# Performance work log

Measured on AMD Instinct MI355X. Metric: run time of the kernel, lower is better.

## Reference

```python
import jax, jax.numpy as jnp
import numpy as np

EPS = 1e-10


def _log_scaling(feats):
    """Raw feats (..., 15): xmin,ymin,xmax,ymax,area,angle,pca_big,pca_small,hu1..hu7
    -> (..., 17): xmin..area, log|pca_big..hu7|, lshape, cosangle, sinangle."""
    lshape = jnp.sqrt(feats[..., 7:8]) / (jnp.sqrt(feats[..., 6:7]) + EPS)
    cosangle = jnp.cos(feats[..., 5:6])
    sinangle = jnp.sin(feats[..., 5:6])
    logged = jnp.log(jnp.abs(feats[..., 5:]) + EPS)  # cols 5..14 logged
    # original drops the (logged) angle column 5 and keeps logged cols 6..14
    return jnp.concatenate([feats[..., :5], logged[..., 1:], lshape, cosangle, sinangle], axis=-1)


def _make_parents(n_trees, P, seed=0):
    """Valid topologically-ordered tree: parent[p] < p, parent[0] = 0 (root)."""
    rng = np.random.default_rng(seed)
    idx = np.arange(P)
    high = np.maximum(idx, 1)
    par = rng.integers(0, 2**31 - 1, size=(n_trees, P)) % high[None, :]
    par[:, 0] = 0
    return par.astype(np.int32)


def setup_inputs() -> dict:
    key = jax.random.key(0)
    k1, k2, k3, k4 = jax.random.split(key, 4)
    B, N, H, W = 2, 2, 1024, 1024
    P = H * W
    x = jax.random.normal(k1, (B, N, H, W), dtype=jnp.float32) * 10.0
    weight = jax.random.uniform(k2, (N, 17, 1), dtype=jnp.float32, minval=-0.01, maxval=0.01)
    bias = jnp.zeros((N, 1), dtype=jnp.float32)
    attrs = jax.random.uniform(k3, (B, N, P, 15), dtype=jnp.float32) * 4.0
    parents = jnp.asarray(_make_parents(B * N, P).reshape(B, N, P))
    return {"x": x, "weight": weight, "bias": bias, "attrs": attrs, "parents": parents}


def _path_sum(contrib_pad, par_pad, P):
    """Pointer-doubling root-to-node path sums over a tree with sentinel at index P."""
    iters = max(int(np.ceil(np.log2(max(P, 2)))), 1)

    def body(i, carry):
        v, p = carry
        return v + v[p], p[p]

    v, _ = jax.lax.fori_loop(0, iters, body, (contrib_pad, par_pad))
    return v[:P]


def reference(x, weight, bias, attrs, parents):
    B, N, H, W = x.shape
    P = H * W
    xf = x.reshape(B, N, P)
    idx = jnp.arange(P, dtype=parents.dtype)
    is_root = parents == idx  # (B,N,P)
    parent_vals = jnp.take_along_axis(xf, parents, axis=-1)
    diff = jnp.where(is_root, xf, xf - parent_vals)  # per-node gray-level increment
    feats = _log_scaling(attrs)  # (B,N,P,17)
    lin = jnp.einsum('bnpf,nfo->bnpo', feats, weight) + bias[None, :, None, :]
    scores = jax.nn.sigmoid(lin[..., 0])  # (B,N,P)
    contrib = diff * scores
    # sentinel node P with contribution 0; roots point at the sentinel
    sent = jnp.full((B, N, 1), P, dtype=parents.dtype)
    par_pad = jnp.concatenate([jnp.where(is_root, P, parents), sent], axis=-1)
    contrib_pad = jnp.concatenate([contrib, jnp.zeros((B, N, 1), x.dtype)], axis=-1)
    out = jax.vmap(jax.vmap(lambda c, p: _path_sum(c, p, P)))(contrib_pad, par_pad)
    return out.reshape(B, N, H, W)
```

## Files before the change

### kernel.cpp

```cpp
#include <hip/hip_runtime.h>
#include <math.h>

#define EPSF 1e-10f
#define P_NODES (1 << 20)
#define T_FRONT 65536
#define T_C1    262144
#define T_C2    524288

typedef float vf4 __attribute__((ext_vector_type(4)));
typedef float vf2 __attribute__((ext_vector_type(2)));

struct __align__(8) NodePair {
    float v;
    int   par;
};

__device__ __forceinline__ void tree_decomp(int b, int& tree, int& jj)
{
    tree = (b & 7) >> 1;
    jj   = ((b >> 3) << 1) | (b & 1);
}

__global__ __launch_bounds__(256) void score_kernel(
    const float* __restrict__ x,
    const float* __restrict__ weight,
    const float* __restrict__ bias,
    const float* __restrict__ attrs,
    const int*   __restrict__ parents,
    NodePair*    __restrict__ dst,
    int N)
{
    __shared__ float sA[256 * 15];

    const int t = threadIdx.x;
    int tree, jj;
    tree_decomp(blockIdx.x, tree, jj);
    const int blockBase = (tree << 20) + (jj << 8);
    const int idx = blockBase + t;

    const vf4* ab4 = (const vf4*)(attrs + (size_t)blockBase * 15);
    vf4* sA4 = (vf4*)sA;
#pragma unroll
    for (int k = t; k < 960; k += 256)
        sA4[k] = __builtin_nontemporal_load(&ab4[k]);

    const int n    = tree % N;
    const float* w = weight + n * 17;
    const float  b = bias[n];

    __syncthreads();

    const float* a = &sA[t * 15];

    float acc = b;
    acc += a[0] * w[0];
    acc += a[1] * w[1];
    acc += a[2] * w[2];
    acc += a[3] * w[3];
    acc += a[4] * w[4];

    const float a5 = a[5];
    const float a6 = a[6];
    const float a7 = a[7];

    acc += __logf(fabsf(a6)    + EPSF) * w[5];
    acc += __logf(fabsf(a7)    + EPSF) * w[6];
    acc += __logf(fabsf(a[8])  + EPSF) * w[7];
    acc += __logf(fabsf(a[9])  + EPSF) * w[8];
    acc += __logf(fabsf(a[10]) + EPSF) * w[9];
    acc += __logf(fabsf(a[11]) + EPSF) * w[10];
    acc += __logf(fabsf(a[12]) + EPSF) * w[11];
    acc += __logf(fabsf(a[13]) + EPSF) * w[12];
    acc += __logf(fabsf(a[14]) + EPSF) * w[13];

    const float lshape = __fsqrt_rn(a7) / (__fsqrt_rn(a6) + EPSF);
    acc += lshape * w[14];
    acc += __cosf(a5) * w[15];
    acc += __sinf(a5) * w[16];

    const float score = 1.0f / (1.0f + __expf(-acc));

    const int   p   = idx & (P_NODES - 1);
    const int   par = parents[idx];
    const float xv  = x[idx];

    NodePair r;
    if (par == p) {
        r.v   = xv * score;
        r.par = -1;
    } else {
        r.v   = (xv - x[(idx - p) + par]) * score;
        r.par = par;
    }
    dst[idx] = r;
}

__global__ __launch_bounds__(256) void frontier_kernel(
    const NodePair* __restrict__ pairs,
    float*          __restrict__ out)
{
    int tree, jj;
    tree_decomp(blockIdx.x, tree, jj);
    const int p    = (jj << 8) + threadIdx.x;
    const int base = tree << 20;
    const NodePair* tp = pairs + base;

    NodePair r = tp[p];
    float s = r.v;
    int   c = r.par;
    while (c >= 0) {
        NodePair q = tp[c];
        s += q.v;
        c  = q.par;
    }
    out[base + p] = s;
}

__global__ __launch_bounds__(256) void chunk_kernel(
    const NodePair* __restrict__ pairs,
    float*          __restrict__ out,
    int lo, int last)
{
    int tree, jj;
    tree_decomp(blockIdx.x, tree, jj);
    const int p0   = lo + ((((jj << 8) + threadIdx.x)) << 1);
    const int base = tree << 20;
    const NodePair* tp = pairs + base;

    float4 r = *(const float4*)(tp + p0);
    float s0 = r.x;  int c0 = __float_as_int(r.y);
    float s1 = r.z;  int c1 = __float_as_int(r.w);

    bool a0 = (c0 >= lo), a1 = (c1 >= lo);
    while (a0 || a1) {
        NodePair q0, q1;
        if (a0) q0 = tp[c0];
        if (a1) q1 = tp[c1];
        if (a0) { s0 += q0.v; c0 = q0.par; a0 = (c0 >= lo); }
        if (a1) { s1 += q1.v; c1 = q1.par; a1 = (c1 >= lo); }
    }
    s0 += out[base + c0];
    s1 += out[base + c1];

    vf2 o; o.x = s0; o.y = s1;
    if (last)
        __builtin_nontemporal_store(o, (vf2*)(out + base + p0));
    else
        *(vf2*)(out + base + p0) = o;
}

extern "C" void kernel_launch(void* const* d_in, const int* in_sizes, int n_in,
                              void* d_out, int out_size, void* d_ws, size_t ws_size,
                              hipStream_t stream)
{
    const float* x       = (const float*)d_in[0];
    const float* weight  = (const float*)d_in[1];
    const float* bias    = (const float*)d_in[2];
    const float* attrs   = (const float*)d_in[3];
    const int*   parents = (const int*)d_in[4];
    float*       out     = (float*)d_out;

    const int total  = in_sizes[0];
    const int N      = in_sizes[1] / 17;
    const int nTrees = total >> 20;

    NodePair* pairs = (NodePair*)d_ws;

    const int block = 256;

    score_kernel<<<total / block, block, 0, stream>>>(x, weight, bias, attrs,
                                                      parents, pairs, N);

    frontier_kernel<<<(T_FRONT / block) * nTrees, block, 0, stream>>>(pairs, out);

    chunk_kernel<<<((T_C1 - T_FRONT) / (2 * block)) * nTrees, block, 0, stream>>>(
        pairs, out, T_FRONT, 0);

    chunk_kernel<<<((T_C2 - T_C1) / (2 * block)) * nTrees, block, 0, stream>>>(
        pairs, out, T_C1, 0);

    chunk_kernel<<<((P_NODES - T_C2) / (2 * block)) * nTrees, block, 0, stream>>>(
        pairs, out, T_C2, 1);
}
```

Baseline: 401.2 us.

## Merge path-sum chunk kernels into one cooperative kernel with grid syncs

Replaces the frontier kernel and three chunk launches with a single cooperative kernel of 1024 blocks. It walks a smaller 16K-node frontier, then processes doubling chunks separated by grid-wide syncs, so each chunk's chain walks are shorter. This is meant to remove separate kernel launch overhead and allow finer chunking. The cost is grid-sync latency and persistent-thread loops with less parallelism per phase. The old multi-kernel path is kept as a fallback if the cooperative launch fails.

```diff
diff --git a/kernel.cpp b/kernel.cpp
--- a/kernel.cpp
+++ b/kernel.cpp
@@ -1,11 +1,11 @@
 #include <hip/hip_runtime.h>
+#include <hip/hip_cooperative_groups.h>
 #include <math.h>
+
+namespace cg = cooperative_groups;
 
 #define EPSF 1e-10f
 #define P_NODES (1 << 20)
-#define T_FRONT 65536
-#define T_C1    262144
-#define T_C2    524288
 
 typedef float vf4 __attribute__((ext_vector_type(4)));
 typedef float vf2 __attribute__((ext_vector_type(2)));
@@ -95,16 +95,8 @@
     dst[idx] = r;
 }
 
-__global__ __launch_bounds__(256) void frontier_kernel(
-    const NodePair* __restrict__ pairs,
-    float*          __restrict__ out)
-{
-    int tree, jj;
-    tree_decomp(blockIdx.x, tree, jj);
-    const int p    = (jj << 8) + threadIdx.x;
-    const int base = tree << 20;
-    const NodePair* tp = pairs + base;
-
+__device__ __forceinline__ float full_walk(const NodePair* __restrict__ tp, int p)
+{
     NodePair r = tp[p];
     float s = r.v;
     int   c = r.par;
@@ -113,7 +105,73 @@
         s += q.v;
         c  = q.par;
     }
-    out[base + p] = s;
+    return s;
+}
+
+__device__ __forceinline__ void chunk_span(
+    const NodePair* __restrict__ tp, float* __restrict__ to,
+    int tid, int tstride, int lo, int hi, int last)
+{
+    for (int p0 = lo + (tid << 1); p0 < hi; p0 += (tstride << 1)) {
+        float4 r = *(const float4*)(tp + p0);
+        float s0 = r.x;  int c0 = __float_as_int(r.y);
+        float s1 = r.z;  int c1 = __float_as_int(r.w);
+
+        bool a0 = (c0 >= lo), a1 = (c1 >= lo);
+        while (a0 || a1) {
+            NodePair q0, q1;
+            if (a0) q0 = tp[c0];
+            if (a1) q1 = tp[c1];
+            if (a0) { s0 += q0.v; c0 = q0.par; a0 = (c0 >= lo); }
+            if (a1) { s1 += q1.v; c1 = q1.par; a1 = (c1 >= lo); }
+        }
+        s0 += to[c0];
+        s1 += to[c1];
+
+        vf2 o; o.x = s0; o.y = s1;
+        if (last)
+            __builtin_nontemporal_store(o, (vf2*)(to + p0));
+        else
+            *(vf2*)(to + p0) = o;
+    }
+}
+
+#define CHAIN_BLOCKS 1024
+
+__global__ __launch_bounds__(256) void chain_all_kernel(
+    const NodePair* __restrict__ pairs,
+    float*          __restrict__ out)
+{
+    cg::grid_group grid = cg::this_grid();
+
+    int tree, jj;
+    tree_decomp(blockIdx.x, tree, jj);
+    const int tpt  = (CHAIN_BLOCKS / 4) * 256;
+    const int tid  = (jj << 8) + threadIdx.x;
+    const NodePair* tp = pairs + (tree << 20);
+    float*          to = out   + (tree << 20);
+
+    for (int p = tid; p < (16 << 10); p += tpt)
+        to[p] = full_walk(tp, p);
+    grid.sync();
+
+    chunk_span(tp, to, tid, tpt,  16 << 10,   32 << 10, 0); grid.sync();
+    chunk_span(tp, to, tid, tpt,  32 << 10,   64 << 10, 0); grid.sync();
+    chunk_span(tp, to, tid, tpt,  64 << 10,  128 << 10, 0); grid.sync();
+    chunk_span(tp, to, tid, tpt, 128 << 10,  256 << 10, 0); grid.sync();
+    chunk_span(tp, to, tid, tpt, 256 << 10,  512 << 10, 0); grid.sync();
+    chunk_span(tp, to, tid, tpt, 512 << 10, 1024 << 10, 1);
+}
+
+__global__ __launch_bounds__(256) void frontier_kernel(
+    const NodePair* __restrict__ pairs,
+    float*          __restrict__ out)
+{
+    int tree, jj;
+    tree_decomp(blockIdx.x, tree, jj);
+    const int p    = (jj << 8) + threadIdx.x;
+    const int base = tree << 20;
+    out[base + p] = full_walk(pairs + base, p);
 }
 
 __global__ __launch_bounds__(256) void chunk_kernel(
@@ -126,6 +184,7 @@
     const int p0   = lo + ((((jj << 8) + threadIdx.x)) << 1);
     const int base = tree << 20;
     const NodePair* tp = pairs + base;
+    float*          to = out + base;
 
     float4 r = *(const float4*)(tp + p0);
     float s0 = r.x;  int c0 = __float_as_int(r.y);
@@ -139,14 +198,14 @@
         if (a0) { s0 += q0.v; c0 = q0.par; a0 = (c0 >= lo); }
         if (a1) { s1 += q1.v; c1 = q1.par; a1 = (c1 >= lo); }
     }
-    s0 += out[base + c0];
-    s1 += out[base + c1];
+    s0 += to[c0];
+    s1 += to[c1];
 
     vf2 o; o.x = s0; o.y = s1;
     if (last)
-        __builtin_nontemporal_store(o, (vf2*)(out + base + p0));
+        __builtin_nontemporal_store(o, (vf2*)(to + p0));
     else
-        *(vf2*)(out + base + p0) = o;
+        *(vf2*)(to + p0) = o;
 }
 
 extern "C" void kernel_launch(void* const* d_in, const int* in_sizes, int n_in,
@@ -171,14 +230,22 @@
     score_kernel<<<total / block, block, 0, stream>>>(x, weight, bias, attrs,
                                                       parents, pairs, N);
 
-    frontier_kernel<<<(T_FRONT / block) * nTrees, block, 0, stream>>>(pairs, out);
-
-    chunk_kernel<<<((T_C1 - T_FRONT) / (2 * block)) * nTrees, block, 0, stream>>>(
-        pairs, out, T_FRONT, 0);
-
-    chunk_kernel<<<((T_C2 - T_C1) / (2 * block)) * nTrees, block, 0, stream>>>(
-        pairs, out, T_C1, 0);
-
-    chunk_kernel<<<((P_NODES - T_C2) / (2 * block)) * nTrees, block, 0, stream>>>(
-        pairs, out, T_C2, 1);
-}
+    bool coop_ok = false;
+    if (nTrees == 4) {
+        void* args[2] = { (void*)&pairs, (void*)&out };
+        hipError_t e = hipLaunchCooperativeKernel((void*)chain_all_kernel,
+                                                  dim3(CHAIN_BLOCKS), dim3(block),
+                                                  args, 0, stream);
+        coop_ok = (e == hipSuccess);
+    }
+
+    if (!coop_ok) {
+        frontier_kernel<<<(65536 / block) * nTrees, block, 0, stream>>>(pairs, out);
+        const int bounds[4] = { 65536, 262144, 524288, 1048576 };
+        for (int i = 0; i < 3; ++i) {
+            int lo = bounds[i], hi = bounds[i + 1];
+            int g  = ((hi - lo) / (2 * block)) * nTrees;
+            chunk_kernel<<<g, block, 0, stream>>>(pairs, out, lo, i == 2);
+        }
+    }
+}
```

After: 1.109 ms. +176.3%, slower.

## Chase eight pointer chains per thread and rebalance chunk boundaries

Applied to the files above, without the earlier changes.

The chunk kernel now has each thread follow eight independent ancestor chains at once instead of two, so more memory loads are in flight per thread and the latency of dependent pointer chasing is hidden better. The frontier is shrunk to the first 16K nodes and the chunk split points are moved, so the later chunks use shorter chains and the naive frontier walk does less work. The cost is fewer threads in flight, higher register pressure, and waves that stay busy until their longest of eight chains finishes.

```diff
diff --git a/kernel.cpp b/kernel.cpp
--- a/kernel.cpp
+++ b/kernel.cpp
@@ -3,9 +3,9 @@
 
 #define EPSF 1e-10f
 #define P_NODES (1 << 20)
-#define T_FRONT 65536
-#define T_C1    262144
-#define T_C2    524288
+#define T_F  16384
+#define T_C0 65536
+#define T_C1 262144
 
 typedef float vf4 __attribute__((ext_vector_type(4)));
 typedef float vf2 __attribute__((ext_vector_type(2)));
@@ -116,37 +116,75 @@
     out[base + p] = s;
 }
 
-__global__ __launch_bounds__(256) void chunk_kernel(
+__global__ __launch_bounds__(256) void chunk8_kernel(
     const NodePair* __restrict__ pairs,
     float*          __restrict__ out,
     int lo, int last)
 {
     int tree, jj;
     tree_decomp(blockIdx.x, tree, jj);
-    const int p0   = lo + ((((jj << 8) + threadIdx.x)) << 1);
     const int base = tree << 20;
     const NodePair* tp = pairs + base;
-
-    float4 r = *(const float4*)(tp + p0);
-    float s0 = r.x;  int c0 = __float_as_int(r.y);
-    float s1 = r.z;  int c1 = __float_as_int(r.w);
-
-    bool a0 = (c0 >= lo), a1 = (c1 >= lo);
-    while (a0 || a1) {
-        NodePair q0, q1;
+    float*          to = out + base;
+    const int S = lo + jj * 2048 + (threadIdx.x << 1);
+
+    float4 r0 = *(const float4*)(tp + S);
+    float4 r1 = *(const float4*)(tp + S + 512);
+    float4 r2 = *(const float4*)(tp + S + 1024);
+    float4 r3 = *(const float4*)(tp + S + 1536);
+
+    float s0 = r0.x; int c0 = __float_as_int(r0.y);
+    float s1 = r0.z; int c1 = __float_as_int(r0.w);
+    float s2 = r1.x; int c2 = __float_as_int(r1.y);
+    float s3 = r1.z; int c3 = __float_as_int(r1.w);
+    float s4 = r2.x; int c4 = __float_as_int(r2.y);
+    float s5 = r2.z; int c5 = __float_as_int(r2.w);
+    float s6 = r3.x; int c6 = __float_as_int(r3.y);
+    float s7 = r3.z; int c7 = __float_as_int(r3.w);
+
+    bool a0 = (c0 >= lo), a1 = (c1 >= lo), a2 = (c2 >= lo), a3 = (c3 >= lo);
+    bool a4 = (c4 >= lo), a5 = (c5 >= lo), a6 = (c6 >= lo), a7 = (c7 >= lo);
+
+    while (a0 | a1 | a2 | a3 | a4 | a5 | a6 | a7) {
+        NodePair q0, q1, q2, q3, q4, q5, q6, q7;
         if (a0) q0 = tp[c0];
         if (a1) q1 = tp[c1];
+        if (a2) q2 = tp[c2];
+        if (a3) q3 = tp[c3];
+        if (a4) q4 = tp[c4];
+        if (a5) q5 = tp[c5];
+        if (a6) q6 = tp[c6];
+        if (a7) q7 = tp[c7];
         if (a0) { s0 += q0.v; c0 = q0.par; a0 = (c0 >= lo); }
         if (a1) { s1 += q1.v; c1 = q1.par; a1 = (c1 >= lo); }
-    }
-    s0 += out[base + c0];
-    s1 += out[base + c1];
-
-    vf2 o; o.x = s0; o.y = s1;
-    if (last)
-        __builtin_nontemporal_store(o, (vf2*)(out + base + p0));
-    else
-        *(vf2*)(out + base + p0) = o;
+        if (a2) { s2 += q2.v; c2 = q2.par; a2 = (c2 >= lo); }
+        if (a3) { s3 += q3.v; c3 = q3.par; a3 = (c3 >= lo); }
+        if (a4) { s4 += q4.v; c4 = q4.par; a4 = (c4 >= lo); }
+        if (a5) { s5 += q5.v; c5 = q5.par; a5 = (c5 >= lo); }
+        if (a6) { s6 += q6.v; c6 = q6.par; a6 = (c6 >= lo); }
+        if (a7) { s7 += q7.v; c7 = q7.par; a7 = (c7 >= lo); }
+    }
+
+    float o0 = to[c0], o1 = to[c1], o2 = to[c2], o3 = to[c3];
+    float o4 = to[c4], o5 = to[c5], o6 = to[c6], o7 = to[c7];
+    s0 += o0; s1 += o1; s2 += o2; s3 += o3;
+    s4 += o4; s5 += o5; s6 += o6; s7 += o7;
+
+    vf2 w0; w0.x = s0; w0.y = s1;
+    vf2 w1; w1.x = s2; w1.y = s3;
+    vf2 w2; w2.x = s4; w2.y = s5;
+    vf2 w3; w3.x = s6; w3.y = s7;
+    if (last) {
+        __builtin_nontemporal_store(w0, (vf2*)(to + S));
+        __builtin_nontemporal_store(w1, (vf2*)(to + S + 512));
+        __builtin_nontemporal_store(w2, (vf2*)(to + S + 1024));
+        __builtin_nontemporal_store(w3, (vf2*)(to + S + 1536));
+    } else {
+        *(vf2*)(to + S)        = w0;
+        *(vf2*)(to + S + 512)  = w1;
+        *(vf2*)(to + S + 1024) = w2;
+        *(vf2*)(to + S + 1536) = w3;
+    }
 }
 
 extern "C" void kernel_launch(void* const* d_in, const int* in_sizes, int n_in,
@@ -171,14 +209,14 @@
     score_kernel<<<total / block, block, 0, stream>>>(x, weight, bias, attrs,
                                                       parents, pairs, N);
 
-    frontier_kernel<<<(T_FRONT / block) * nTrees, block, 0, stream>>>(pairs, out);
-
-    chunk_kernel<<<((T_C1 - T_FRONT) / (2 * block)) * nTrees, block, 0, stream>>>(
-        pairs, out, T_FRONT, 0);
-
-    chunk_kernel<<<((T_C2 - T_C1) / (2 * block)) * nTrees, block, 0, stream>>>(
-        pairs, out, T_C1, 0);
-
-    chunk_kernel<<<((P_NODES - T_C2) / (2 * block)) * nTrees, block, 0, stream>>>(
-        pairs, out, T_C2, 1);
-}
+    frontier_kernel<<<(T_F / block) * nTrees, block, 0, stream>>>(pairs, out);
+
+    chunk8_kernel<<<((T_C0 - T_F) / 2048) * nTrees, block, 0, stream>>>(
+        pairs, out, T_F, 0);
+
+    chunk8_kernel<<<((T_C1 - T_C0) / 2048) * nTrees, block, 0, stream>>>(
+        pairs, out, T_C0, 0);
+
+    chunk8_kernel<<<((P_NODES - T_C1) / 2048) * nTrees, block, 0, stream>>>(
+        pairs, out, T_C1, 1);
+}
```

Result: slower. 416.5 us (+3.8%).

## Restructure tree path-sum into doubling chunk passes with 8 chains per thread

Applied to the files above, without the earlier changes.

The score kernel now stores x, score and parent in a 16-byte record and no longer gathers the parent's x. The parent difference is computed on the fly during each chain walk. The frontier shrinks to 4096 nodes, and the rest of each tree is handled by a sequence of doubling-range chunk kernels. Each thread walks 8 independent chains to expose memory-level parallelism, and a separate (x, out) buffer resolves chain ends below the chunk boundary. This trades wider records, extra workspace and more kernel launches (some with very few blocks) for shorter chains and no random gather in the score pass.

```diff
diff --git a/kernel.cpp b/kernel.cpp
--- a/kernel.cpp
+++ b/kernel.cpp
@@ -3,17 +3,11 @@
 
 #define EPSF 1e-10f
 #define P_NODES (1 << 20)
-#define T_FRONT 65536
-#define T_C1    262144
-#define T_C2    524288
+#define T_F 4096
 
 typedef float vf4 __attribute__((ext_vector_type(4)));
 typedef float vf2 __attribute__((ext_vector_type(2)));
 
-struct __align__(8) NodePair {
-    float v;
-    int   par;
-};
 
 __device__ __forceinline__ void tree_decomp(int b, int& tree, int& jj)
 {
@@ -27,7 +21,7 @@
     const float* __restrict__ bias,
     const float* __restrict__ attrs,
     const int*   __restrict__ parents,
-    NodePair*    __restrict__ dst,
+    float4*      __restrict__ rec,
     int N)
 {
     __shared__ float sA[256 * 15];
@@ -80,73 +74,128 @@
 
     const float score = 1.0f / (1.0f + __expf(-acc));
 
-    const int   p   = idx & (P_NODES - 1);
-    const int   par = parents[idx];
-    const float xv  = x[idx];
-
-    NodePair r;
-    if (par == p) {
-        r.v   = xv * score;
-        r.par = -1;
-    } else {
-        r.v   = (xv - x[(idx - p) + par]) * score;
-        r.par = par;
-    }
-    dst[idx] = r;
+    const int p   = idx & (P_NODES - 1);
+    const int par = parents[idx];
+
+    float4 r;
+    r.x = x[idx];
+    r.y = score;
+    r.z = __int_as_float(par == p ? -1 : par);
+    r.w = 0.0f;
+    rec[idx] = r;
 }
 
 __global__ __launch_bounds__(256) void frontier_kernel(
-    const NodePair* __restrict__ pairs,
-    float*          __restrict__ out)
+    const float4* __restrict__ rec,
+    float2*       __restrict__ fin2,
+    float*        __restrict__ out)
 {
     int tree, jj;
     tree_decomp(blockIdx.x, tree, jj);
     const int p    = (jj << 8) + threadIdx.x;
     const int base = tree << 20;
-    const NodePair* tp = pairs + base;
-
-    NodePair r = tp[p];
-    float s = r.v;
-    int   c = r.par;
+    const float4* tp = rec + base;
+
+    float4 r = tp[p];
+    const float ox = r.x;
+    float s  = 0.0f;
+    float cx = r.x, csc = r.y;
+    int   c  = __float_as_int(r.z);
     while (c >= 0) {
-        NodePair q = tp[c];
-        s += q.v;
-        c  = q.par;
-    }
-    out[base + p] = s;
-}
-
-__global__ __launch_bounds__(256) void chunk_kernel(
-    const NodePair* __restrict__ pairs,
-    float*          __restrict__ out,
+        float4 q = tp[c];
+        s  += (cx - q.x) * csc;
+        cx  = q.x; csc = q.y;
+        c   = __float_as_int(q.z);
+    }
+    s += cx * csc;
+
+    __builtin_nontemporal_store(s, out + base + p);
+    vf2 f; f.x = ox; f.y = s;
+    *(vf2*)(fin2 + base + p) = f;
+}
+
+#define CHAIN_STEP(K)                                                        \
+    if (a##K) {                                                              \
+        float4 q = tp[c##K];                                                 \
+        s##K  += (cx##K - q.x) * sc##K;                                      \
+        cx##K  = q.x; sc##K = q.y;                                           \
+        c##K   = __float_as_int(q.z);                                        \
+        a##K   = (c##K >= lo);                                               \
+    }
+
+__global__ __launch_bounds__(256) void chunk8_kernel(
+    const float4* __restrict__ rec,
+    float2*       __restrict__ fin2,
+    float*        __restrict__ out,
     int lo, int last)
 {
     int tree, jj;
     tree_decomp(blockIdx.x, tree, jj);
-    const int p0   = lo + ((((jj << 8) + threadIdx.x)) << 1);
     const int base = tree << 20;
-    const NodePair* tp = pairs + base;
-
-    float4 r = *(const float4*)(tp + p0);
-    float s0 = r.x;  int c0 = __float_as_int(r.y);
-    float s1 = r.z;  int c1 = __float_as_int(r.w);
-
-    bool a0 = (c0 >= lo), a1 = (c1 >= lo);
-    while (a0 || a1) {
-        NodePair q0, q1;
-        if (a0) q0 = tp[c0];
-        if (a1) q1 = tp[c1];
-        if (a0) { s0 += q0.v; c0 = q0.par; a0 = (c0 >= lo); }
-        if (a1) { s1 += q1.v; c1 = q1.par; a1 = (c1 >= lo); }
-    }
-    s0 += out[base + c0];
-    s1 += out[base + c1];
-
-    vf2 o; o.x = s0; o.y = s1;
-    if (last)
-        __builtin_nontemporal_store(o, (vf2*)(out + base + p0));
-    else
-        *(vf2*)(out + base + p0) = o;
+    const float4* tp = rec  + base;
+    float2*       tf = fin2 + base;
+    float*        to = out  + base;
+    const int S = lo + jj * 2048 + threadIdx.x;
+
+    float4 r0 = tp[S];
+    float4 r1 = tp[S +  256];
+    float4 r2 = tp[S +  512];
+    float4 r3 = tp[S +  768];
+    float4 r4 = tp[S + 1024];
+    float4 r5 = tp[S + 1280];
+    float4 r6 = tp[S + 1536];
+    float4 r7 = tp[S + 1792];
+
+    float ox0 = r0.x, cx0 = r0.x, sc0 = r0.y; int c0 = __float_as_int(r0.z);
+    float ox1 = r1.x, cx1 = r1.x, sc1 = r1.y; int c1 = __float_as_int(r1.z);
+    float ox2 = r2.x, cx2 = r2.x, sc2 = r2.y; int c2 = __float_as_int(r2.z);
+    float ox3 = r3.x, cx3 = r3.x, sc3 = r3.y; int c3 = __float_as_int(r3.z);
+    float ox4 = r4.x, cx4 = r4.x, sc4 = r4.y; int c4 = __float_as_int(r4.z);
+    float ox5 = r5.x, cx5 = r5.x, sc5 = r5.y; int c5 = __float_as_int(r5.z);
+    float ox6 = r6.x, cx6 = r6.x, sc6 = r6.y; int c6 = __float_as_int(r6.z);
+    float ox7 = r7.x, cx7 = r7.x, sc7 = r7.y; int c7 = __float_as_int(r7.z);
+
+    float s0 = 0.f, s1 = 0.f, s2 = 0.f, s3 = 0.f;
+    float s4 = 0.f, s5 = 0.f, s6 = 0.f, s7 = 0.f;
+
+    bool a0 = (c0 >= lo), a1 = (c1 >= lo), a2 = (c2 >= lo), a3 = (c3 >= lo);
+    bool a4 = (c4 >= lo), a5 = (c5 >= lo), a6 = (c6 >= lo), a7 = (c7 >= lo);
+
+    while (a0 | a1 | a2 | a3 | a4 | a5 | a6 | a7) {
+        CHAIN_STEP(0) CHAIN_STEP(1) CHAIN_STEP(2) CHAIN_STEP(3)
+        CHAIN_STEP(4) CHAIN_STEP(5) CHAIN_STEP(6) CHAIN_STEP(7)
+    }
+
+    float2 f0 = tf[c0], f1 = tf[c1], f2 = tf[c2], f3 = tf[c3];
+    float2 f4 = tf[c4], f5 = tf[c5], f6 = tf[c6], f7 = tf[c7];
+    s0 += (cx0 - f0.x) * sc0 + f0.y;
+    s1 += (cx1 - f1.x) * sc1 + f1.y;
+    s2 += (cx2 - f2.x) * sc2 + f2.y;
+    s3 += (cx3 - f3.x) * sc3 + f3.y;
+    s4 += (cx4 - f4.x) * sc4 + f4.y;
+    s5 += (cx5 - f5.x) * sc5 + f5.y;
+    s6 += (cx6 - f6.x) * sc6 + f6.y;
+    s7 += (cx7 - f7.x) * sc7 + f7.y;
+
+    __builtin_nontemporal_store(s0, to + S);
+    __builtin_nontemporal_store(s1, to + S +  256);
+    __builtin_nontemporal_store(s2, to + S +  512);
+    __builtin_nontemporal_store(s3, to + S +  768);
+    __builtin_nontemporal_store(s4, to + S + 1024);
+    __builtin_nontemporal_store(s5, to + S + 1280);
+    __builtin_nontemporal_store(s6, to + S + 1536);
+    __builtin_nontemporal_store(s7, to + S + 1792);
+
+    if (!last) {
+        vf2 g0; g0.x = ox0; g0.y = s0; *(vf2*)(tf + S)        = g0;
+        vf2 g1; g1.x = ox1; g1.y = s1; *(vf2*)(tf + S +  256) = g1;
+        vf2 g2; g2.x = ox2; g2.y = s2; *(vf2*)(tf + S +  512) = g2;
+        vf2 g3; g3.x = ox3; g3.y = s3; *(vf2*)(tf + S +  768) = g3;
+        vf2 g4; g4.x = ox4; g4.y = s4; *(vf2*)(tf + S + 1024) = g4;
+        vf2 g5; g5.x = ox5; g5.y = s5; *(vf2*)(tf + S + 1280) = g5;
+        vf2 g6; g6.x = ox6; g6.y = s6; *(vf2*)(tf + S + 1536) = g6;
+        vf2 g7; g7.x = ox7; g7.y = s7; *(vf2*)(tf + S + 1792) = g7;
+    }
 }
 
 extern "C" void kernel_launch(void* const* d_in, const int* in_sizes, int n_in,
@@ -164,21 +213,20 @@
     const int N      = in_sizes[1] / 17;
     const int nTrees = total >> 20;
 
-    NodePair* pairs = (NodePair*)d_ws;
+    float4* rec  = (float4*)d_ws;
+    float2* fin2 = (float2*)((char*)d_ws + ((size_t)total * 16));
 
     const int block = 256;
 
     score_kernel<<<total / block, block, 0, stream>>>(x, weight, bias, attrs,
-                                                      parents, pairs, N);
-
-    frontier_kernel<<<(T_FRONT / block) * nTrees, block, 0, stream>>>(pairs, out);
-
-    chunk_kernel<<<((T_C1 - T_FRONT) / (2 * block)) * nTrees, block, 0, stream>>>(
-        pairs, out, T_FRONT, 0);
-
-    chunk_kernel<<<((T_C2 - T_C1) / (2 * block)) * nTrees, block, 0, stream>>>(
-        pairs, out, T_C1, 0);
-
-    chunk_kernel<<<((P_NODES - T_C2) / (2 * block)) * nTrees, block, 0, stream>>>(
-        pairs, out, T_C2, 1);
-}
+                                                      parents, rec, N);
+
+    frontier_kernel<<<(T_F / block) * nTrees, block, 0, stream>>>(rec, fin2, out);
+
+    for (int lo = T_F; lo < P_NODES; lo <<= 1) {
+        const int span = lo;
+        const int last = (lo << 1) >= P_NODES;
+        chunk8_kernel<<<(span / 2048) * nTrees, block, 0, stream>>>(
+            rec, fin2, out, lo, last);
+    }
+}
```

Result: slower. 451.4 us (+12.5%).
